# Kernel optimization log

Hardware: AMD Instinct MI355X
Metric: run time of the kernel (lower is better)

## Reference

```python
import jax, jax.numpy as jnp
import numpy as np

SR = 16000
NYQ = SR / 2.0
N_FFT = 400
HOP = 160
WIN = 400
OUT_CHANNELS = 64
OUTPUT_SIZE = 64
MIN_LOW_HZ = 50.0
MIN_BAND_HZ = 50.0
FRAME_LENGTH = 400
EPS_LN = 1e-5


def _to_mel(hz):
    return 2595.0 * np.log10(1.0 + hz / 700.0)


def _to_hz(mel):
    return 700.0 * (10.0 ** (mel / 2595.0) - 1.0)


def setup_inputs() -> dict:
    key = jax.random.key(0)
    k1, = jax.random.split(key, 1)
    waveforms = jax.random.normal(k1, (1024, 1, 16000), dtype=jnp.float32)
    # mel-spaced init, exactly as in __init__ (freq_init='mel', range_constraint=False)
    low_hz = 30.0
    high_hz = NYQ - (MIN_LOW_HZ + MIN_BAND_HZ)
    mel = np.linspace(_to_mel(low_hz), _to_mel(high_hz), OUT_CHANNELS + 1)
    hz = _to_hz(mel)
    low_hz_ = jnp.asarray(hz[:-1], dtype=jnp.float32).reshape(-1, 1)
    band_hz_ = jnp.asarray(np.diff(hz), dtype=jnp.float32).reshape(-1, 1)
    ln_weight = jnp.ones((OUT_CHANNELS, 1), dtype=jnp.float32)
    ln_bias = jnp.zeros((OUT_CHANNELS, 1), dtype=jnp.float32)
    return {
        "waveforms": waveforms,
        "low_hz_": low_hz_,
        "band_hz_": band_hz_,
        "ln_weight": ln_weight,
        "ln_bias": ln_bias,
    }


def _hann_periodic(n):
    # torch.hann_window default: periodic=True
    k = jnp.arange(n, dtype=jnp.float32)
    return 0.5 - 0.5 * jnp.cos(2.0 * jnp.pi * k / n)


def _stft_mag(x):
    pad = N_FFT // 2
    xp = jnp.pad(x, ((0, 0), (pad, pad)), mode="reflect")
    n_frames = 1 + (xp.shape[1] - N_FFT) // HOP
    idx = jnp.arange(n_frames)[:, None] * HOP + jnp.arange(N_FFT)[None, :]
    frames = xp[:, idx] * _hann_periodic(WIN)  # [B, F_t, n_fft]
    spec = jnp.fft.rfft(frames, axis=-1)       # [B, F_t, n_fft//2+1]
    return jnp.abs(spec).transpose(0, 2, 1)    # [B, n_fft//2+1, F_t]


def _get_filters(low_hz_, band_hz_):
    # vectorized over all channels (original loops per channel)
    low = MIN_LOW_HZ + jnp.abs(low_hz_)                                   # [C,1]
    high = jnp.clip(low + MIN_BAND_HZ + jnp.abs(band_hz_), MIN_LOW_HZ, NYQ)
    freq = jnp.linspace(0.0, NYQ, N_FFT // 2 + 1, dtype=jnp.float32)      # [F]
    mask = (freq >= low) & (freq <= high)                                 # [C,F]
    center = (low + high) / 2.0
    bw = high - low
    resp = 1.0 - jnp.abs(freq - center) / (bw / 2.0)                      # triangular
    return jnp.where(mask, resp, 0.0)                                     # [C,F]


def _gln(x, weight, bias):
    # GlobalLayerNorm over dims (1,2) of [B,C,T]
    mean = jnp.mean(x, axis=(1, 2), keepdims=True)
    var = jnp.mean((x - mean) ** 2, axis=(1, 2), keepdims=True)
    return weight * (x - mean) / jnp.sqrt(var + EPS_LN) + bias


def _interp_linear(x, out_size):
    # torch F.interpolate(mode='linear', align_corners=False) along last dim
    t_in = x.shape[-1]
    scale = t_in / out_size
    pos = (jnp.arange(out_size, dtype=jnp.float32) + 0.5) * scale - 0.5
    pos = jnp.clip(pos, 0.0, t_in - 1)
    i0 = jnp.floor(pos).astype(jnp.int32)
    i1 = jnp.minimum(i0 + 1, t_in - 1)
    w = (pos - i0.astype(jnp.float32))
    return x[..., i0] * (1.0 - w) + x[..., i1] * w


def reference(waveforms, low_hz_, band_hz_, ln_weight, ln_bias):
    B = waveforms.shape[0]
    target_length = HOP * (OUTPUT_SIZE - 1) + FRAME_LENGTH  # 10480
    cur = waveforms.shape[-1]
    x = waveforms[:, 0, :]
    if target_length > cur:  # static shape decision
        x = jnp.pad(x, ((0, 0), (0, target_length - cur)))
    mag_spec = _stft_mag(x)                       # [B, 201, F_t]
    filters = _get_filters(low_hz_, band_hz_)     # [C, 201]
    filtered = jnp.einsum("cf,bft->bct", filters, mag_spec)  # [B, C, F_t]
    filtered = _gln(filtered, ln_weight, ln_bias)
    energy = filtered ** 2
    log_energy = jnp.log10(energy + 1e-6)         # [B, C, F_t]
    if log_energy.shape[-1] != OUTPUT_SIZE:
        log_energy = _interp_linear(log_energy, OUTPUT_SIZE)  # [B, C, 64]
    log_energy = log_energy[:, None, :, :].transpose(0, 1, 3, 2)  # [B,1,64,C]
    return (log_energy, filters)
```

## Files before the change

kernel.cpp:

```cpp
#include <hip/hip_runtime.h>
#include <math.h>

#define BLOCK 512
#define MSTR 209

typedef __attribute__((ext_vector_type(8))) short short8;
typedef __attribute__((ext_vector_type(16))) float f32x16;
typedef __attribute__((ext_vector_type(8))) float f32x8;

__device__ inline unsigned short f2bf(float x) {
    unsigned u = __float_as_uint(x);
    unsigned r = u + 0x7fffu + ((u >> 16) & 1u);
    return (unsigned short)(r >> 16);
}

struct ASplit { short8 h, l; };

__device__ inline ASplit splitA(f32x8 v) {
    unsigned ah[4], al[4];
    #pragma unroll
    for (int q = 0; q < 4; ++q) {
        unsigned short h0 = f2bf(v[2*q]),   h1 = f2bf(v[2*q+1]);
        float hf0 = __uint_as_float((unsigned)h0 << 16);
        float hf1 = __uint_as_float((unsigned)h1 << 16);
        unsigned short l0 = f2bf(v[2*q] - hf0), l1 = f2bf(v[2*q+1] - hf1);
        ah[q] = (unsigned)h0 | ((unsigned)h1 << 16);
        al[q] = (unsigned)l0 | ((unsigned)l1 << 16);
    }
    ASplit r;
    r.h = __builtin_bit_cast(short8, *(uint4*)ah);
    r.l = __builtin_bit_cast(short8, *(uint4*)al);
    return r;
}

__device__ inline f32x8 loadA8(const float* __restrict__ x, int i0) {
    f32x8 r;
    if (i0 >= 0 && i0 <= 15992) {
        float4 a0 = *(const float4*)(x + i0);
        float4 a1 = *(const float4*)(x + i0 + 4);
        r[0] = a0.x; r[1] = a0.y; r[2] = a0.z; r[3] = a0.w;
        r[4] = a1.x; r[5] = a1.y; r[6] = a1.z; r[7] = a1.w;
    } else {
        #pragma unroll
        for (int e = 0; e < 8; ++e) {
            int p = i0 + e;
            p = (p < 0) ? -p : p;
            p = (p > 15999) ? (31998 - p) : p;
            r[e] = x[p];
        }
    }
    return r;
}

__global__ void fse_filters(const float* __restrict__ low_hz_,
                            const float* __restrict__ band_hz_,
                            float* __restrict__ out)
{
    int idx = blockIdx.x * 256 + threadIdx.x;
    if (idx >= 64 * 201) return;
    int c = idx / 201;
    int k = idx - c * 201;
    float lo = 50.0f + fabsf(low_hz_[c]);
    float hi = lo + 50.0f + fabsf(band_hz_[c]);
    hi = fminf(fmaxf(hi, 50.0f), 8000.0f);
    float ctr = 0.5f * (lo + hi);
    float hbw = 0.5f * (hi - lo);
    float fq = 40.0f * (float)k;
    float resp = 1.0f - fabsf(fq - ctr) / hbw;
    out[idx] = (fq >= lo && fq <= hi) ? resp : 0.0f;
}

__global__ void fse_setup_B(unsigned short* __restrict__ bt)
{
    int idx = blockIdx.x * 256 + threadIdx.x;
    if (idx >= 372736) return;
    int e   = idx & 7;
    int t   = idx >> 3;
    int row = t % 448;
    int q   = t / 448;
    int p   = q & 3;
    int pl  = (q >> 2) & 1;
    int kc  = q >> 3;
    int n   = kc * 32 + p * 8 + e;
    float v = 0.0f;
    if (n < 400) {
        int bin = -1, isim = 0;
        if (row <= 200) bin = row;
        else if (row >= 224 && row <= 424) { bin = row - 224; isim = 1; }
        if (bin >= 0) {
            int a = (bin * n) % 400;
            float th = 6.283185307179586f * ((float)a / 400.0f);
            float sn, cs;
            sincosf(th, &sn, &cs);
            float wn = 0.5f - 0.5f * cosf(6.283185307179586f * ((float)n / 400.0f));
            v = isim ? (-wn * sn) : (wn * cs);
        }
    }
    unsigned short h = f2bf(v);
    float hf = __uint_as_float((unsigned)h << 16);
    unsigned short l = f2bf(v - hf);
    bt[idx] = pl ? l : h;
}

__global__ __launch_bounds__(512, 2)
void fse_main_mfma(const float* __restrict__ wav,
                   const float* __restrict__ low_hz_,
                   const float* __restrict__ band_hz_,
                   const float* __restrict__ ln_w,
                   const float* __restrict__ ln_b,
                   const unsigned short* __restrict__ Bt,
                   float* __restrict__ out)
{
    __shared__ __align__(16) char smem[114688];
    float* mags = (float*)smem;
    float* fbuf = (float*)(smem + 84544);

    __shared__ float fctr[64], finv[64];
    __shared__ int   fks[64], fke[64];
    __shared__ float red[16];
    __shared__ float stats[2];

    const int b    = blockIdx.x;
    const int tid  = threadIdx.x;
    const int w    = tid >> 6;
    const int lane = tid & 63;
    const float* __restrict__ x = wav + b * 16000;

    if (tid < 64) {
        float lo = 50.0f + fabsf(low_hz_[tid]);
        float hi = lo + 50.0f + fabsf(band_hz_[tid]);
        hi = fminf(fmaxf(hi, 50.0f), 8000.0f);
        float ctr = 0.5f * (lo + hi);
        float hbw = 0.5f * (hi - lo);
        int ks = (int)ceilf(lo * 0.025f);
        if (ks < 0) ks = 0;
        while (40.0f * (float)ks < lo) ++ks;
        while (ks > 0 && 40.0f * (float)(ks - 1) >= lo) --ks;
        int ke = (int)floorf(hi * 0.025f);
        if (ke > 200) ke = 200;
        while (40.0f * (float)ke > hi) --ke;
        while (ke < 200 && 40.0f * (float)(ke + 1) <= hi) ++ke;
        fctr[tid] = ctr;
        finv[tid] = (hbw > 0.0f) ? (1.0f / hbw) : 0.0f;
        fks[tid]  = ks;
        fke[tid]  = ke;
    }

    const int mt   = w >> 1;
    const int half = w & 1;
    const int jrow = lane & 31;
    const int g    = lane >> 5;
    const int arow = mt * 32 + jrow;
    const int te   = (arow <= 100) ? arow : 50;
    const int abase = 160 * te - 200 + g * 8;

    const uint4* __restrict__ btg = (const uint4*)Bt;

    f32x8 ac0 = loadA8(x, abase);
    f32x8 ac1 = loadA8(x, abase + 16);
    {
        uint4 rr0 = btg[0 * 512 + tid], rr1 = btg[1 * 512 + tid];
        uint4 rr2 = btg[2 * 512 + tid], rr3 = btg[3 * 512 + tid];
        uint4 rr4 = btg[4 * 512 + tid], rr5 = btg[5 * 512 + tid];
        uint4 rr6 = btg[6 * 512 + tid];
        uint4* dst = (uint4*)smem;
        dst[0 * 512 + tid] = rr0; dst[1 * 512 + tid] = rr1;
        dst[2 * 512 + tid] = rr2; dst[3 * 512 + tid] = rr3;
        dst[4 * 512 + tid] = rr4; dst[5 * 512 + tid] = rr5;
        dst[6 * 512 + tid] = rr6;
    }
    __syncthreads();

    f32x16 acc[7];
    #pragma unroll
    for (int n = 0; n < 7; ++n) {
        #pragma unroll
        for (int e = 0; e < 16; ++e) acc[n][e] = 0.0f;
    }

    int curoff = 0;
    for (int kc = 0; kc < 13; ++kc) {
        const bool pre = (kc < 12);
        uint4 rr0, rr1, rr2, rr3, rr4, rr5, rr6;
        f32x8 an0, an1;
        if (pre) {
            const uint4* src = btg + (kc + 1) * 3584;
            rr0 = src[0 * 512 + tid]; rr1 = src[1 * 512 + tid];
            rr2 = src[2 * 512 + tid]; rr3 = src[3 * 512 + tid];
            rr4 = src[4 * 512 + tid]; rr5 = src[5 * 512 + tid];
            rr6 = src[6 * 512 + tid];
            an0 = loadA8(x, abase + (kc + 1) * 32);
            an1 = loadA8(x, abase + (kc + 1) * 32 + 16);
        }

        ASplit A0 = splitA(ac0);
        ASplit A1 = splitA(ac1);

        const unsigned short* bs = (const unsigned short*)(smem + curoff);
        #pragma unroll
        for (int s = 0; s < 2; ++s) {
            const short8 Ah = s ? A1.h : A0.h;
            const short8 Al = s ? A1.l : A0.l;
            const int pb = (s * 2 + g) * 448;
            #pragma unroll
            for (int n = 0; n < 7; ++n) {
                const int ro = (half * 7 + n) * 32 + jrow;
                short8 Bh = *(const short8*)(bs + (pb + ro) * 8);
                short8 Bl = *(const short8*)(bs + 14336 + (pb + ro) * 8);
                acc[n] = __builtin_amdgcn_mfma_f32_32x32x16_bf16(Ah, Bh, acc[n], 0, 0, 0);
                acc[n] = __builtin_amdgcn_mfma_f32_32x32x16_bf16(Ah, Bl, acc[n], 0, 0, 0);
                acc[n] = __builtin_amdgcn_mfma_f32_32x32x16_bf16(Al, Bh, acc[n], 0, 0, 0);
            }
        }

        if (pre) {
            uint4* dst = (uint4*)(smem + (curoff ^ 57344));
            dst[0 * 512 + tid] = rr0; dst[1 * 512 + tid] = rr1;
            dst[2 * 512 + tid] = rr2; dst[3 * 512 + tid] = rr3;
            dst[4 * 512 + tid] = rr4; dst[5 * 512 + tid] = rr5;
            dst[6 * 512 + tid] = rr6;
        }
        __syncthreads();
        if (pre) { ac0 = an0; ac1 = an1; }
        curoff ^= 57344;
    }

    if (half == 0) {
        #pragma unroll
        for (int n = 0; n < 7; ++n) {
            int k = n * 32 + jrow;
            if (k <= 200) {
                #pragma unroll
                for (int r = 0; r < 16; ++r) {
                    int t = mt * 32 + (r & 3) + 8 * (r >> 2) + 4 * g;
                    if (t <= 100) mags[t * MSTR + k] = acc[n][r];
                }
            }
        }
    }
    __syncthreads();
    if (half == 1) {
        #pragma unroll
        for (int n = 0; n < 7; ++n) {
            int k = n * 32 + jrow;
            if (k <= 200) {
                #pragma unroll
                for (int r = 0; r < 16; ++r) {
                    int t = mt * 32 + (r & 3) + 8 * (r >> 2) + 4 * g;
                    if (t <= 100) {
                        float re = mags[t * MSTR + k];
                        float im = acc[n][r];
                        mags[t * MSTR + k] = sqrtf(re * re + im * im);
                    }
                }
            }
        }
    }
    __syncthreads();

    {
        const int t0 = lane;
        const int t1v = 64 + lane;
        const int t1 = (t1v <= 100) ? t1v : 100;
        #pragma unroll
        for (int i = 0; i < 8; ++i) {
            const int c = w * 8 + i;
            const float ctr = fctr[c];
            const float inv = finv[c];
            const int ks = fks[c], ke = fke[c];
            float a0 = 0.0f, a1 = 0.0f;
            for (int k = ks; k <= ke; ++k) {
                float resp = 1.0f - fabsf(40.0f * (float)k - ctr) * inv;
                a0 = fmaf(resp, mags[t0 * MSTR + k], a0);
                a1 = fmaf(resp, mags[t1 * MSTR + k], a1);
            }
            fbuf[c * 101 + t0] = a0;
            if (t1v <= 100) fbuf[c * 101 + t1v] = a1;
        }
    }
    __syncthreads();

    float s = 0.0f, ss = 0.0f;
    for (int i = tid; i < 6464; i += BLOCK) {
        float vv = fbuf[i];
        s += vv;
        ss = fmaf(vv, vv, ss);
    }
    #pragma unroll
    for (int off = 32; off > 0; off >>= 1) {
        s  += __shfl_down(s,  off, 64);
        ss += __shfl_down(ss, off, 64);
    }
    if (lane == 0) { red[w] = s; red[8 + w] = ss; }
    __syncthreads();
    if (tid == 0) {
        float ts = 0.0f, tss = 0.0f;
        for (int i = 0; i < 8; ++i) { ts += red[i]; tss += red[8 + i]; }
        float mu = ts * (1.0f / 6464.0f);
        stats[0] = mu;
        stats[1] = tss * (1.0f / 6464.0f) - mu * mu;
    }
    __syncthreads();
    const float mu   = stats[0];
    const float isig = 1.0f / sqrtf(stats[1] + 1e-5f);

    for (int idx = tid; idx < 4096; idx += BLOCK) {
        const int to = idx >> 6;
        const int c  = idx & 63;
        float pos = ((float)to + 0.5f) * 1.578125f - 0.5f;
        pos = fminf(fmaxf(pos, 0.0f), 100.0f);
        int i0 = (int)floorf(pos);
        int i1 = i0 + 1; if (i1 > 100) i1 = 100;
        float fr = pos - (float)i0;
        float wc = ln_w[c], bc = ln_b[c];
        float x0 = fbuf[c * 101 + i0];
        float x1 = fbuf[c * 101 + i1];
        float y0 = fmaf(wc, (x0 - mu) * isig, bc);
        float y1 = fmaf(wc, (x1 - mu) * isig, bc);
        float l0 = log10f(fmaf(y0, y0, 1e-6f));
        float l1 = log10f(fmaf(y1, y1, 1e-6f));
        out[b * 4096 + idx] = l0 * (1.0f - fr) + l1 * fr;
    }
}

__global__ __launch_bounds__(512, 2)
void fse_main_valu(const float* __restrict__ wav,
                   const float* __restrict__ low_hz_,
                   const float* __restrict__ band_hz_,
                   const float* __restrict__ ln_w,
                   const float* __restrict__ ln_b,
                   float* __restrict__ out)
{
    __shared__ float  xp[16400];
    __shared__ float2 Xs[8][204];
    __shared__ float  mags[8][204];
    __shared__ float  fbuf[64 * 101];
    __shared__ float  fctr[64], finv[64];
    __shared__ int    fks[64], fke[64];
    __shared__ float  red[8];
    __shared__ float  stats[2];

    const int b    = blockIdx.x;
    const int tid  = threadIdx.x;
    const int w    = tid >> 6;
    const int lane = tid & 63;
    const float* __restrict__ x = wav + b * 16000;

    for (int i = tid; i < 16400; i += BLOCK) {
        int p = i - 200;
        p = (p < 0) ? -p : p;
        p = (p > 15999) ? (31998 - p) : p;
        xp[i] = x[p];
    }
    if (tid < 64) {
        float lo = 50.0f + fabsf(low_hz_[tid]);
        float hi = lo + 50.0f + fabsf(band_hz_[tid]);
        hi = fminf(fmaxf(hi, 50.0f), 8000.0f);
        float ctr = 0.5f * (lo + hi);
        float hbw = 0.5f * (hi - lo);
        int ks = (int)ceilf(lo * 0.025f);
        if (ks < 0) ks = 0;
        while (40.0f * (float)ks < lo) ++ks;
        while (ks > 0 && 40.0f * (float)(ks - 1) >= lo) --ks;
        int ke = (int)floorf(hi * 0.025f);
        if (ke > 200) ke = 200;
        while (40.0f * (float)ke > hi) --ke;
        while (ke < 200 && 40.0f * (float)(ke + 1) <= hi) ++ke;
        fctr[tid] = ctr;
        finv[tid] = (hbw > 0.0f) ? (1.0f / hbw) : 0.0f;
        fks[tid]  = ks;
        fke[tid]  = ke;
    }
    __syncthreads();

    const float cctr = fctr[lane];
    const float cinv = finv[lane];
    const int   cks  = fks[lane];
    const int   cke  = fke[lane];

    float reX[4][13], imX[4][13];
    const float2* __restrict__ xp2 = (const float2*)xp;
    float c0[4], s0[4], c1[4], s1[4], cd[4], sd[4];
    #pragma unroll
    for (int m = 0; m < 4; ++m) {
        const int k = m * 64 + lane;
        const float th = -0.015707963267948966f * (float)k;
        sincosf(th, &s1[m], &c1[m]);
        sincosf(th + th, &sd[m], &cd[m]);
        c0[m] = 1.0f; s0[m] = 0.0f;
        #pragma unroll
        for (int j = 0; j < 13; ++j) { reX[m][j] = 0.0f; imX[m][j] = 0.0f; }
    }
    const int o12 = (w < 5) ? 640 * 12 : 0;
    int ib = 80 * w;
    #pragma unroll 2
    for (int h = 0; h < 200; ++h) {
        #pragma unroll
        for (int j = 0; j < 13; ++j) {
            const int off = (j == 12) ? o12 : 640 * j;
            float2 f = xp2[ib + off];
            #pragma unroll
            for (int m = 0; m < 4; ++m) {
                reX[m][j] = fmaf(f.x, c0[m], reX[m][j]);
                imX[m][j] = fmaf(f.x, s0[m], imX[m][j]);
                reX[m][j] = fmaf(f.y, c1[m], reX[m][j]);
                imX[m][j] = fmaf(f.y, s1[m], imX[m][j]);
            }
        }
        #pragma unroll
        for (int m = 0; m < 4; ++m) {
            float nc0 = fmaf(c0[m], cd[m], -(s0[m] * sd[m]));
            float ns0 = fmaf(s0[m], cd[m],  (c0[m] * sd[m]));
            float nc1 = fmaf(c1[m], cd[m], -(s1[m] * sd[m]));
            float ns1 = fmaf(s1[m], cd[m],  (c1[m] * sd[m]));
            c0[m] = nc0; s0[m] = ns0; c1[m] = nc1; s1[m] = ns1;
        }
        ++ib;
    }

    float2* __restrict__ myX   = &Xs[w][0];
    float*  __restrict__ mymag = &mags[w][0];
    for (int j = 0; j < 13; ++j) {
        const int t = w + 8 * j;
        if (t > 100) break;
        #pragma unroll
        for (int m = 0; m < 4; ++m) {
            const int k = m * 64 + lane;
            if (k < 202) myX[k] = make_float2(reX[m][j], imX[m][j]);
        }
        asm volatile("s_waitcnt lgkmcnt(0)" ::: "memory");
        #pragma unroll
        for (int m = 0; m < 4; ++m) {
            const int k = m * 64 + lane;
            if (k <= 200) {
                float2 xm = (k == 0) ? myX[1] : myX[k - 1];
                float imm = (k == 0) ? -xm.y : xm.y;
                float2 xq = myX[k + 1];
                float rw = 0.5f * reX[m][j] - 0.25f * (xm.x + xq.x);
                float iw = 0.5f * imX[m][j] - 0.25f * (imm  + xq.y);
                mymag[k] = sqrtf(rw * rw + iw * iw);
            }
        }
        asm volatile("s_waitcnt lgkmcnt(0)" ::: "memory");
        float acc = 0.0f;
        for (int k = cks; k <= cke; ++k) {
            float resp = 1.0f - fabsf(40.0f * (float)k - cctr) * cinv;
            acc = fmaf(resp, mymag[k], acc);
        }
        fbuf[lane * 101 + t] = acc;
    }
    __syncthreads();

    float s = 0.0f;
    for (int i = tid; i < 6464; i += BLOCK) s += fbuf[i];
    #pragma unroll
    for (int off = 32; off > 0; off >>= 1) s += __shfl_down(s, off, 64);
    if (lane == 0) red[w] = s;
    __syncthreads();
    if (tid == 0) {
        float tsum = 0.0f;
        for (int i = 0; i < 8; ++i) tsum += red[i];
        stats[0] = tsum * (1.0f / 6464.0f);
    }
    __syncthreads();
    const float mu = stats[0];
    float v = 0.0f;
    for (int i = tid; i < 6464; i += BLOCK) { float d = fbuf[i] - mu; v = fmaf(d, d, v); }
    #pragma unroll
    for (int off = 32; off > 0; off >>= 1) v += __shfl_down(v, off, 64);
    if (lane == 0) red[w] = v;
    __syncthreads();
    if (tid == 0) {
        float tsum = 0.0f;
        for (int i = 0; i < 8; ++i) tsum += red[i];
        stats[1] = tsum * (1.0f / 6464.0f);
    }
    __syncthreads();
    const float var  = stats[1];
    const float isig = 1.0f / sqrtf(var + 1e-5f);

    for (int idx = tid; idx < 4096; idx += BLOCK) {
        const int to = idx >> 6;
        const int c  = idx & 63;
        float pos = ((float)to + 0.5f) * 1.578125f - 0.5f;
        pos = fminf(fmaxf(pos, 0.0f), 100.0f);
        int i0 = (int)floorf(pos);
        int i1 = i0 + 1; if (i1 > 100) i1 = 100;
        float fr = pos - (float)i0;
        float wc = ln_w[c], bc = ln_b[c];
        float x0 = fbuf[c * 101 + i0];
        float x1 = fbuf[c * 101 + i1];
        float y0 = fmaf(wc, (x0 - mu) * isig, bc);
        float y1 = fmaf(wc, (x1 - mu) * isig, bc);
        float l0 = log10f(fmaf(y0, y0, 1e-6f));
        float l1 = log10f(fmaf(y1, y1, 1e-6f));
        out[b * 4096 + idx] = l0 * (1.0f - fr) + l1 * fr;
    }
}

extern "C" void kernel_launch(void* const* d_in, const int* in_sizes, int n_in,
                              void* d_out, int out_size, void* d_ws, size_t ws_size,
                              hipStream_t stream)
{
    const float* wav = (const float*)d_in[0];
    const float* lo  = (const float*)d_in[1];
    const float* bd  = (const float*)d_in[2];
    const float* lw  = (const float*)d_in[3];
    const float* lb  = (const float*)d_in[4];
    float* out = (float*)d_out;

    fse_filters<<<(64 * 201 + 255) / 256, 256, 0, stream>>>(lo, bd, out + 1024 * 4096);

    const size_t BNEED = (size_t)372736 * sizeof(unsigned short);
    if (ws_size >= BNEED) {
        unsigned short* Bts = (unsigned short*)d_ws;
        fse_setup_B<<<(372736 + 255) / 256, 256, 0, stream>>>(Bts);
        fse_main_mfma<<<1024, BLOCK, 0, stream>>>(wav, lo, bd, lw, lb, Bts, out);
    } else {
        fse_main_valu<<<1024, BLOCK, 0, stream>>>(wav, lo, bd, lw, lb, out);
    }
}
```

Baseline: 231.7 us.

## Read DFT basis directly from global memory with 2x4 wave tiling, dropping LDS staging

Replaces the double-buffered LDS staging of the bf16 DFT basis with direct global (L2-cached) loads of B fragments. Work is re-tiled so each wave computes two 32-row M tiles across 3-4 N tiles, which reuses every B fragment twice and removes the per-chunk barriers. The shared-memory footprint shrinks to the mags and fbuf arrays. The cost is that B loads now go to global memory inside the MFMA loop with no prefetching, so latency may be exposed, and load balance across waves is uneven.

```diff
diff --git a/kernel.cpp b/kernel.cpp
--- a/kernel.cpp
+++ b/kernel.cpp
@@ -111,10 +111,8 @@
                    const unsigned short* __restrict__ Bt,
                    float* __restrict__ out)
 {
-    __shared__ __align__(16) char smem[114688];
-    float* mags = (float*)smem;
-    float* fbuf = (float*)(smem + 84544);
-
+    __shared__ float mags[101 * MSTR];
+    __shared__ float fbuf[64 * 101];
     __shared__ float fctr[64], finv[64];
     __shared__ int   fks[64], fke[64];
     __shared__ float red[16];
@@ -146,111 +144,101 @@
         fke[tid]  = ke;
     }
 
-    const int mt   = w >> 1;
-    const int half = w & 1;
-    const int jrow = lane & 31;
-    const int g    = lane >> 5;
-    const int arow = mt * 32 + jrow;
-    const int te   = (arow <= 100) ? arow : 50;
-    const int abase = 160 * te - 200 + g * 8;
-
-    const uint4* __restrict__ btg = (const uint4*)Bt;
-
-    f32x8 ac0 = loadA8(x, abase);
-    f32x8 ac1 = loadA8(x, abase + 16);
-    {
-        uint4 rr0 = btg[0 * 512 + tid], rr1 = btg[1 * 512 + tid];
-        uint4 rr2 = btg[2 * 512 + tid], rr3 = btg[3 * 512 + tid];
-        uint4 rr4 = btg[4 * 512 + tid], rr5 = btg[5 * 512 + tid];
-        uint4 rr6 = btg[6 * 512 + tid];
-        uint4* dst = (uint4*)smem;
-        dst[0 * 512 + tid] = rr0; dst[1 * 512 + tid] = rr1;
-        dst[2 * 512 + tid] = rr2; dst[3 * 512 + tid] = rr3;
-        dst[4 * 512 + tid] = rr4; dst[5 * 512 + tid] = rr5;
-        dst[6 * 512 + tid] = rr6;
-    }
-    __syncthreads();
-
-    f32x16 acc[7];
-    #pragma unroll
-    for (int n = 0; n < 7; ++n) {
-        #pragma unroll
-        for (int e = 0; e < 16; ++e) acc[n][e] = 0.0f;
-    }
-
-    int curoff = 0;
+    const int mg    = w >> 2;
+    const int nq    = w & 3;
+    const int nbase = (nq < 3) ? nq * 4 : 11;
+    const int cnt   = (nq < 2) ? 4 : 3;
+    const int jrow  = lane & 31;
+    const int g     = lane >> 5;
+
+    const int arow0 = 64 * mg + jrow;
+    const int arow1 = 64 * mg + 32 + jrow;
+    const int te0   = (arow0 <= 100) ? arow0 : 50;
+    const int te1   = (arow1 <= 100) ? arow1 : 50;
+    const int ab0   = 160 * te0 - 200 + g * 8;
+    const int ab1   = 160 * te1 - 200 + g * 8;
+
+    f32x16 accA[4], accB[4];
+    #pragma unroll
+    for (int n = 0; n < 4; ++n) {
+        #pragma unroll
+        for (int e = 0; e < 16; ++e) { accA[n][e] = 0.0f; accB[n][e] = 0.0f; }
+    }
+
     for (int kc = 0; kc < 13; ++kc) {
-        const bool pre = (kc < 12);
-        uint4 rr0, rr1, rr2, rr3, rr4, rr5, rr6;
-        f32x8 an0, an1;
-        if (pre) {
-            const uint4* src = btg + (kc + 1) * 3584;
-            rr0 = src[0 * 512 + tid]; rr1 = src[1 * 512 + tid];
-            rr2 = src[2 * 512 + tid]; rr3 = src[3 * 512 + tid];
-            rr4 = src[4 * 512 + tid]; rr5 = src[5 * 512 + tid];
-            rr6 = src[6 * 512 + tid];
-            an0 = loadA8(x, abase + (kc + 1) * 32);
-            an1 = loadA8(x, abase + (kc + 1) * 32 + 16);
-        }
-
-        ASplit A0 = splitA(ac0);
-        ASplit A1 = splitA(ac1);
-
-        const unsigned short* bs = (const unsigned short*)(smem + curoff);
+        f32x8 a00 = loadA8(x, ab0 + kc * 32);
+        f32x8 a01 = loadA8(x, ab0 + kc * 32 + 16);
+        f32x8 a10 = loadA8(x, ab1 + kc * 32);
+        f32x8 a11 = loadA8(x, ab1 + kc * 32 + 16);
+        ASplit A00 = splitA(a00);
+        ASplit A01 = splitA(a01);
+        ASplit A10 = splitA(a10);
+        ASplit A11 = splitA(a11);
+
         #pragma unroll
         for (int s = 0; s < 2; ++s) {
-            const short8 Ah = s ? A1.h : A0.h;
-            const short8 Al = s ? A1.l : A0.l;
-            const int pb = (s * 2 + g) * 448;
+            const short8 Ah0 = s ? A01.h : A00.h;
+            const short8 Al0 = s ? A01.l : A00.l;
+            const short8 Ah1 = s ? A11.h : A10.h;
+            const short8 Al1 = s ? A11.l : A10.l;
+            const int part = s * 2 + g;
+            const int bh = ((kc * 2 + 0) * 4 + part) * 3584;
+            const int bl = ((kc * 2 + 1) * 4 + part) * 3584;
             #pragma unroll
-            for (int n = 0; n < 7; ++n) {
-                const int ro = (half * 7 + n) * 32 + jrow;
-                short8 Bh = *(const short8*)(bs + (pb + ro) * 8);
-                short8 Bl = *(const short8*)(bs + 14336 + (pb + ro) * 8);
-                acc[n] = __builtin_amdgcn_mfma_f32_32x32x16_bf16(Ah, Bh, acc[n], 0, 0, 0);
-                acc[n] = __builtin_amdgcn_mfma_f32_32x32x16_bf16(Ah, Bl, acc[n], 0, 0, 0);
-                acc[n] = __builtin_amdgcn_mfma_f32_32x32x16_bf16(Al, Bh, acc[n], 0, 0, 0);
-            }
-        }
-
-        if (pre) {
-            uint4* dst = (uint4*)(smem + (curoff ^ 57344));
-            dst[0 * 512 + tid] = rr0; dst[1 * 512 + tid] = rr1;
-            dst[2 * 512 + tid] = rr2; dst[3 * 512 + tid] = rr3;
-            dst[4 * 512 + tid] = rr4; dst[5 * 512 + tid] = rr5;
-            dst[6 * 512 + tid] = rr6;
-        }
-        __syncthreads();
-        if (pre) { ac0 = an0; ac1 = an1; }
-        curoff ^= 57344;
-    }
-
-    if (half == 0) {
-        #pragma unroll
-        for (int n = 0; n < 7; ++n) {
-            int k = n * 32 + jrow;
-            if (k <= 200) {
-                #pragma unroll
-                for (int r = 0; r < 16; ++r) {
-                    int t = mt * 32 + (r & 3) + 8 * (r >> 2) + 4 * g;
-                    if (t <= 100) mags[t * MSTR + k] = acc[n][r];
+            for (int n = 0; n < 4; ++n) {
+                if (n < cnt) {
+                    const int ro = (nbase + n) * 32 + jrow;
+                    short8 Bh = *(const short8*)(Bt + bh + ro * 8);
+                    short8 Bl = *(const short8*)(Bt + bl + ro * 8);
+                    accA[n] = __builtin_amdgcn_mfma_f32_32x32x16_bf16(Ah0, Bh, accA[n], 0, 0, 0);
+                    accA[n] = __builtin_amdgcn_mfma_f32_32x32x16_bf16(Ah0, Bl, accA[n], 0, 0, 0);
+                    accA[n] = __builtin_amdgcn_mfma_f32_32x32x16_bf16(Al0, Bh, accA[n], 0, 0, 0);
+                    accB[n] = __builtin_amdgcn_mfma_f32_32x32x16_bf16(Ah1, Bh, accB[n], 0, 0, 0);
+                    accB[n] = __builtin_amdgcn_mfma_f32_32x32x16_bf16(Ah1, Bl, accB[n], 0, 0, 0);
+                    accB[n] = __builtin_amdgcn_mfma_f32_32x32x16_bf16(Al1, Bh, accB[n], 0, 0, 0);
                 }
             }
         }
     }
-    __syncthreads();
-    if (half == 1) {
-        #pragma unroll
-        for (int n = 0; n < 7; ++n) {
-            int k = n * 32 + jrow;
-            if (k <= 200) {
-                #pragma unroll
-                for (int r = 0; r < 16; ++r) {
-                    int t = mt * 32 + (r & 3) + 8 * (r >> 2) + 4 * g;
-                    if (t <= 100) {
-                        float re = mags[t * MSTR + k];
-                        float im = acc[n][r];
-                        mags[t * MSTR + k] = sqrtf(re * re + im * im);
+
+    #pragma unroll
+    for (int n = 0; n < 4; ++n) {
+        if (n < cnt) {
+            const int nt = nbase + n;
+            if (nt < 7) {
+                const int k = nt * 32 + jrow;
+                if (k <= 200) {
+                    #pragma unroll
+                    for (int r = 0; r < 16; ++r) {
+                        int t = 64 * mg + (r & 3) + 8 * (r >> 2) + 4 * g;
+                        if (t <= 100)      mags[t * MSTR + k]        = accA[n][r];
+                        if (t + 32 <= 100) mags[(t + 32) * MSTR + k] = accB[n][r];
+                    }
+                }
+            }
+        }
+    }
+    __syncthreads();
+    #pragma unroll
+    for (int n = 0; n < 4; ++n) {
+        if (n < cnt) {
+            const int nt = nbase + n;
+            if (nt >= 7 && nt < 14) {
+                const int k = (nt - 7) * 32 + jrow;
+                if (k <= 200) {
+                    #pragma unroll
+                    for (int r = 0; r < 16; ++r) {
+                        int t = 64 * mg + (r & 3) + 8 * (r >> 2) + 4 * g;
+                        if (t <= 100) {
+                            float re = mags[t * MSTR + k];
+                            float im = accA[n][r];
+                            mags[t * MSTR + k] = sqrtf(re * re + im * im);
+                        }
+                        if (t + 32 <= 100) {
+                            float re = mags[(t + 32) * MSTR + k];
+                            float im = accB[n][r];
+                            mags[(t + 32) * MSTR + k] = sqrtf(re * re + im * im);
+                        }
                     }
                 }
             }
```

Result: slower. 277.5 us (+19.8%).

## Retile MFMA warps so each computes real and imaginary parts jointly

Applied to the files above, without the earlier changes.

Warps previously each owned one 32-row frame tile and one half (real or imaginary) of all 7 frequency tiles. Now each warp owns two frame tiles and up to two frequency tiles, accumulating both real and imaginary parts in registers. This lets the magnitude be computed directly in registers, removing the shared-memory round trip and the extra barrier between the real and imaginary halves, and reuses each B fragment across two A tiles. The cost is an uneven split of the 7 frequency tiles (2,2,2,1), which gives most warps more MFMAs per step than before, plus twice as many A loads and splits per warp.

```diff
diff --git a/kernel.cpp b/kernel.cpp
--- a/kernel.cpp
+++ b/kernel.cpp
@@ -146,111 +146,132 @@
         fke[tid]  = ke;
     }
 
-    const int mt   = w >> 1;
-    const int half = w & 1;
-    const int jrow = lane & 31;
-    const int g    = lane >> 5;
-    const int arow = mt * 32 + jrow;
-    const int te   = (arow <= 100) ? arow : 50;
-    const int abase = 160 * te - 200 + g * 8;
+    const int mg    = w >> 2;
+    const int pq    = w & 3;
+    const int pbase = pq * 2;
+    const int cnt   = (pq < 3) ? 2 : 1;
+    const int jrow  = lane & 31;
+    const int g     = lane >> 5;
+
+    const int arow0 = 64 * mg + jrow;
+    const int arow1 = 64 * mg + 32 + jrow;
+    const int te0   = (arow0 <= 100) ? arow0 : 50;
+    const int te1   = (arow1 <= 100) ? arow1 : 50;
+    const int ab0   = 160 * te0 - 200 + g * 8;
+    const int ab1   = 160 * te1 - 200 + g * 8;
 
     const uint4* __restrict__ btg = (const uint4*)Bt;
 
-    f32x8 ac0 = loadA8(x, abase);
-    f32x8 ac1 = loadA8(x, abase + 16);
+    f32x8 ac00 = loadA8(x, ab0);
+    f32x8 ac01 = loadA8(x, ab0 + 16);
+    f32x8 ac10 = loadA8(x, ab1);
+    f32x8 ac11 = loadA8(x, ab1 + 16);
     {
-        uint4 rr0 = btg[0 * 512 + tid], rr1 = btg[1 * 512 + tid];
-        uint4 rr2 = btg[2 * 512 + tid], rr3 = btg[3 * 512 + tid];
-        uint4 rr4 = btg[4 * 512 + tid], rr5 = btg[5 * 512 + tid];
-        uint4 rr6 = btg[6 * 512 + tid];
+        uint4 r0 = btg[0 * 512 + tid], r1 = btg[1 * 512 + tid];
+        uint4 r2 = btg[2 * 512 + tid], r3 = btg[3 * 512 + tid];
+        uint4 r4 = btg[4 * 512 + tid], r5 = btg[5 * 512 + tid];
+        uint4 r6 = btg[6 * 512 + tid];
         uint4* dst = (uint4*)smem;
-        dst[0 * 512 + tid] = rr0; dst[1 * 512 + tid] = rr1;
-        dst[2 * 512 + tid] = rr2; dst[3 * 512 + tid] = rr3;
-        dst[4 * 512 + tid] = rr4; dst[5 * 512 + tid] = rr5;
-        dst[6 * 512 + tid] = rr6;
-    }
-    __syncthreads();
-
-    f32x16 acc[7];
-    #pragma unroll
-    for (int n = 0; n < 7; ++n) {
-        #pragma unroll
-        for (int e = 0; e < 16; ++e) acc[n][e] = 0.0f;
-    }
+        dst[0 * 512 + tid] = r0; dst[1 * 512 + tid] = r1;
+        dst[2 * 512 + tid] = r2; dst[3 * 512 + tid] = r3;
+        dst[4 * 512 + tid] = r4; dst[5 * 512 + tid] = r5;
+        dst[6 * 512 + tid] = r6;
+    }
+    __syncthreads();
+
+    f32x16 accR[2][2], accI[2][2];
+    #pragma unroll
+    for (int mt = 0; mt < 2; ++mt)
+        #pragma unroll
+        for (int i = 0; i < 2; ++i)
+            #pragma unroll
+            for (int e = 0; e < 16; ++e) { accR[mt][i][e] = 0.0f; accI[mt][i][e] = 0.0f; }
 
     int curoff = 0;
     for (int kc = 0; kc < 13; ++kc) {
         const bool pre = (kc < 12);
-        uint4 rr0, rr1, rr2, rr3, rr4, rr5, rr6;
-        f32x8 an0, an1;
+
+        ASplit S00 = splitA(ac00);
+        ASplit S01 = splitA(ac01);
+        ASplit S10 = splitA(ac10);
+        ASplit S11 = splitA(ac11);
+
+        uint4 r0, r1, r2, r3, r4, r5, r6;
         if (pre) {
             const uint4* src = btg + (kc + 1) * 3584;
-            rr0 = src[0 * 512 + tid]; rr1 = src[1 * 512 + tid];
-            rr2 = src[2 * 512 + tid]; rr3 = src[3 * 512 + tid];
-            rr4 = src[4 * 512 + tid]; rr5 = src[5 * 512 + tid];
-            rr6 = src[6 * 512 + tid];
-            an0 = loadA8(x, abase + (kc + 1) * 32);
-            an1 = loadA8(x, abase + (kc + 1) * 32 + 16);
-        }
-
-        ASplit A0 = splitA(ac0);
-        ASplit A1 = splitA(ac1);
+            r0 = src[0 * 512 + tid]; r1 = src[1 * 512 + tid];
+            r2 = src[2 * 512 + tid]; r3 = src[3 * 512 + tid];
+            r4 = src[4 * 512 + tid]; r5 = src[5 * 512 + tid];
+            r6 = src[6 * 512 + tid];
+            ac00 = loadA8(x, ab0 + (kc + 1) * 32);
+            ac01 = loadA8(x, ab0 + (kc + 1) * 32 + 16);
+            ac10 = loadA8(x, ab1 + (kc + 1) * 32);
+            ac11 = loadA8(x, ab1 + (kc + 1) * 32 + 16);
+        }
 
         const unsigned short* bs = (const unsigned short*)(smem + curoff);
         #pragma unroll
         for (int s = 0; s < 2; ++s) {
-            const short8 Ah = s ? A1.h : A0.h;
-            const short8 Al = s ? A1.l : A0.l;
-            const int pb = (s * 2 + g) * 448;
+            const short8 Ah0 = s ? S01.h : S00.h;
+            const short8 Al0 = s ? S01.l : S00.l;
+            const short8 Ah1 = s ? S11.h : S10.h;
+            const short8 Al1 = s ? S11.l : S10.l;
+            const int part = s * 2 + g;
+            const int bhof = part * 3584;
+            const int blof = (4 + part) * 3584;
             #pragma unroll
-            for (int n = 0; n < 7; ++n) {
-                const int ro = (half * 7 + n) * 32 + jrow;
-                short8 Bh = *(const short8*)(bs + (pb + ro) * 8);
-                short8 Bl = *(const short8*)(bs + 14336 + (pb + ro) * 8);
-                acc[n] = __builtin_amdgcn_mfma_f32_32x32x16_bf16(Ah, Bh, acc[n], 0, 0, 0);
-                acc[n] = __builtin_amdgcn_mfma_f32_32x32x16_bf16(Ah, Bl, acc[n], 0, 0, 0);
-                acc[n] = __builtin_amdgcn_mfma_f32_32x32x16_bf16(Al, Bh, acc[n], 0, 0, 0);
+            for (int i = 0; i < 2; ++i) {
+                if (i < cnt) {
+                    const int p = pbase + i;
+                    const int roR = p * 32 + jrow;
+                    const int roI = (p + 7) * 32 + jrow;
+                    short8 BhR = *(const short8*)(bs + bhof + roR * 8);
+                    short8 BlR = *(const short8*)(bs + blof + roR * 8);
+                    short8 BhI = *(const short8*)(bs + bhof + roI * 8);
+                    short8 BlI = *(const short8*)(bs + blof + roI * 8);
+                    accR[0][i] = __builtin_amdgcn_mfma_f32_32x32x16_bf16(Ah0, BhR, accR[0][i], 0, 0, 0);
+                    accR[0][i] = __builtin_amdgcn_mfma_f32_32x32x16_bf16(Ah0, BlR, accR[0][i], 0, 0, 0);
+                    accR[0][i] = __builtin_amdgcn_mfma_f32_32x32x16_bf16(Al0, BhR, accR[0][i], 0, 0, 0);
+                    accR[1][i] = __builtin_amdgcn_mfma_f32_32x32x16_bf16(Ah1, BhR, accR[1][i], 0, 0, 0);
+                    accR[1][i] = __builtin_amdgcn_mfma_f32_32x32x16_bf16(Ah1, BlR, accR[1][i], 0, 0, 0);
+                    accR[1][i] = __builtin_amdgcn_mfma_f32_32x32x16_bf16(Al1, BhR, accR[1][i], 0, 0, 0);
+                    accI[0][i] = __builtin_amdgcn_mfma_f32_32x32x16_bf16(Ah0, BhI, accI[0][i], 0, 0, 0);
+                    accI[0][i] = __builtin_amdgcn_mfma_f32_32x32x16_bf16(Ah0, BlI, accI[0][i], 0, 0, 0);
+                    accI[0][i] = __builtin_amdgcn_mfma_f32_32x32x16_bf16(Al0, BhI, accI[0][i], 0, 0, 0);
+                    accI[1][i] = __builtin_amdgcn_mfma_f32_32x32x16_bf16(Ah1, BhI, accI[1][i], 0, 0, 0);
+                    accI[1][i] = __builtin_amdgcn_mfma_f32_32x32x16_bf16(Ah1, BlI, accI[1][i], 0, 0, 0);
+                    accI[1][i] = __builtin_amdgcn_mfma_f32_32x32x16_bf16(Al1, BhI, accI[1][i], 0, 0, 0);
+                }
             }
         }
 
         if (pre) {
             uint4* dst = (uint4*)(smem + (curoff ^ 57344));
-            dst[0 * 512 + tid] = rr0; dst[1 * 512 + tid] = rr1;
-            dst[2 * 512 + tid] = rr2; dst[3 * 512 + tid] = rr3;
-            dst[4 * 512 + tid] = rr4; dst[5 * 512 + tid] = rr5;
-            dst[6 * 512 + tid] = rr6;
+            dst[0 * 512 + tid] = r0; dst[1 * 512 + tid] = r1;
+            dst[2 * 512 + tid] = r2; dst[3 * 512 + tid] = r3;
+            dst[4 * 512 + tid] = r4; dst[5 * 512 + tid] = r5;
+            dst[6 * 512 + tid] = r6;
         }
         __syncthreads();
-        if (pre) { ac0 = an0; ac1 = an1; }
         curoff ^= 57344;
     }
 
-    if (half == 0) {
-        #pragma unroll
-        for (int n = 0; n < 7; ++n) {
-            int k = n * 32 + jrow;
-            if (k <= 200) {
-                #pragma unroll
-                for (int r = 0; r < 16; ++r) {
-                    int t = mt * 32 + (r & 3) + 8 * (r >> 2) + 4 * g;
-                    if (t <= 100) mags[t * MSTR + k] = acc[n][r];
-                }
-            }
-        }
-    }
-    __syncthreads();
-    if (half == 1) {
-        #pragma unroll
-        for (int n = 0; n < 7; ++n) {
-            int k = n * 32 + jrow;
-            if (k <= 200) {
-                #pragma unroll
-                for (int r = 0; r < 16; ++r) {
-                    int t = mt * 32 + (r & 3) + 8 * (r >> 2) + 4 * g;
-                    if (t <= 100) {
-                        float re = mags[t * MSTR + k];
-                        float im = acc[n][r];
-                        mags[t * MSTR + k] = sqrtf(re * re + im * im);
+    #pragma unroll
+    for (int mt = 0; mt < 2; ++mt) {
+        #pragma unroll
+        for (int i = 0; i < 2; ++i) {
+            if (i < cnt) {
+                const int p = pbase + i;
+                const int k = p * 32 + jrow;
+                if (k <= 200) {
+                    #pragma unroll
+                    for (int r = 0; r < 16; ++r) {
+                        int t = 64 * mg + 32 * mt + (r & 3) + 8 * (r >> 2) + 4 * g;
+                        if (t <= 100) {
+                            float re = accR[mt][i][r];
+                            float im = accI[mt][i][r];
+                            mags[t * MSTR + k] = sqrtf(re * re + im * im);
+                        }
                     }
                 }
             }
```

Result: slower. 260.4 us (+12.4%).
